# Kernel optimization log

Hardware: AMD Instinct MI355X
Metric: run time of the kernel (lower is better)

The kernel has to match this reference:

```python
import jax, jax.numpy as jnp
import numpy as np

ALPHA = 0.2  # LeakyReLU slope
NEG_INF = -9e15


def setup_inputs() -> dict:
    key = jax.random.key(0)
    ks = jax.random.split(key, 10)
    N, K, d = 20000, 32, 128
    R, S = 100, 4  # num relations, num domains
    item_embs = jax.random.normal(ks[0], (N, d), dtype=jnp.float32)
    entity_embs = jax.random.normal(ks[1], (N, K, d), dtype=jnp.float32)
    relations_embed = jax.random.normal(ks[2], (N, K, d), dtype=jnp.float32)
    relation_ids = jax.random.randint(ks[3], (N, K), 0, R, dtype=jnp.int32)
    adj_mask = jax.random.randint(ks[4], (N, K), 0, 2, dtype=jnp.int32)
    # fc_attention: Linear(3d, 1); out: Linear(d, d)
    fc_w = jax.random.normal(ks[5], (1, 3 * d), dtype=jnp.float32) * (1.0 / np.sqrt(3 * d))
    fc_b = jnp.zeros((1,), dtype=jnp.float32)
    out_w = jax.random.normal(ks[6], (d, d), dtype=jnp.float32) * (1.0 / np.sqrt(d))
    out_b = jnp.zeros((d,), dtype=jnp.float32)
    rel_dom_probs = jax.nn.softmax(jax.random.normal(ks[7], (R, S), dtype=jnp.float32), axis=-1)
    return {"item_embs": item_embs, "entity_embs": entity_embs,
            "relations_embed": relations_embed, "relation_ids": relation_ids,
            "adj_mask": adj_mask, "fc_w": fc_w, "fc_b": fc_b,
            "out_w": out_w, "out_b": out_b, "rel_dom_probs": rel_dom_probs}


def reference(item_embs, entity_embs, relations_embed, relation_ids, adj_mask,
              fc_w, fc_b, out_w, out_b, rel_dom_probs):
    N, K, d = entity_embs.shape
    R = rel_dom_probs.shape[0]
    # edge attention score: Linear(3d,1) on [item | relation | entity], then LeakyReLU
    Wh = jnp.broadcast_to(item_embs[:, None, :], (N, K, d))
    att_in = jnp.concatenate([Wh, relations_embed, entity_embs], axis=-1)  # [N,K,3d]
    e = jnp.einsum('nkf,of->nk', att_in, fc_w) + fc_b[0]
    e = jnp.where(e > 0, e, ALPHA * e)
    # masked softmax over neighbors (dropout inert in eval)
    masked = jnp.where(adj_mask > 0, e, NEG_INF)
    pi = jax.nn.softmax(masked, axis=1)  # [N,K]
    base = pi[..., None] * relations_embed * entity_embs  # [N,K,d]
    # domain-weighted aggregation: sum_s probs[rel_id, s], invalid ids -> 0
    valid = (relation_ids >= 0) & (relation_ids < R)
    safe_ids = jnp.clip(relation_ids, 0, R - 1)
    a_total = jnp.where(valid, rel_dom_probs[safe_ids].sum(-1), 0.0)  # [N,K]
    agg = jnp.einsum('nk,nkd->nd', a_total, base)  # [N,d]
    # residual + output Linear + ReLU
    out = (agg + item_embs) @ out_w.T + out_b
    return jax.nn.relu(out)
```

## Files before the change

kernel.cpp:

```cpp
#include <hip/hip_runtime.h>

#define ALPHA 0.2f
#define NEG_INF -9e15f

__device__ __forceinline__ void block_bar() {
    asm volatile("s_waitcnt lgkmcnt(0)" ::: "memory");
    __builtin_amdgcn_s_barrier();
}

__device__ __forceinline__ float dot4(float4 a, float4 b) {
    return a.x * b.x + a.y * b.y + a.z * b.z + a.w * b.w;
}

__global__ __launch_bounds__(256, 4)
void gat_k1(const float* __restrict__ item,
            const float* __restrict__ ent,
            const float* __restrict__ rel,
            const int*   __restrict__ rel_ids,
            const int*   __restrict__ adj,
            const float* __restrict__ fc_w,
            const float* __restrict__ fc_b,
            const float* __restrict__ probs,
            float* __restrict__ y,
            int N, int R)
{
    __shared__ __align__(16) float prod[2][4096];
    __shared__ float e_red[32];
    __shared__ float w_lds[32];
    __shared__ float sitem[2];
    __shared__ float asum[128];

    const int t = threadIdx.x;
    const int k = t >> 3, r = t & 7;
    const int base_off = k * 128 + r * 4;

    float4 fr[4], fe[4];
    #pragma unroll
    for (int c = 0; c < 4; ++c) {
        fr[c] = *(const float4*)&fc_w[128 + c * 32 + r * 4];
        fe[c] = *(const float4*)&fc_w[256 + c * 32 + r * 4];
    }
    const float fcw_i = (t < 128) ? fc_w[t] : 0.0f;
    const float fcb   = fc_b[0];
    if (t < R) {
        float4 q = *(const float4*)&probs[t * 4];
        asum[t] = q.x + q.y + q.z + q.w;
    }

    const int stride = gridDim.x;

    float4 pr[4], pe[4];
    float iv_p = 0.0f;
    int mv_p = 0, id_p = 0;
    {
        const float* rp  = rel + (size_t)blockIdx.x * 4096 + base_off;
        const float* epp = ent + (size_t)blockIdx.x * 4096 + base_off;
        #pragma unroll
        for (int c = 0; c < 4; ++c) {
            pr[c] = *(const float4*)(rp  + c * 32);
            pe[c] = *(const float4*)(epp + c * 32);
        }
        if (t < 128) iv_p = item[(size_t)blockIdx.x * 128 + t];
        if (t < 32) {
            mv_p = adj[(size_t)blockIdx.x * 32 + t];
            id_p = rel_ids[(size_t)blockIdx.x * 32 + t];
        }
    }

    int par = 0;
    for (int n = blockIdx.x; n < N; n += stride) {
        const float ivc = iv_p;
        const int mvc = mv_p, idc = id_p;

        float epa = 0.0f;
        float* pb = &prod[par][base_off];
        #pragma unroll
        for (int c = 0; c < 4; ++c) {
            float4 p;
            p.x = pr[c].x * pe[c].x;
            p.y = pr[c].y * pe[c].y;
            p.z = pr[c].z * pe[c].z;
            p.w = pr[c].w * pe[c].w;
            *(float4*)(pb + c * 32) = p;
            epa += dot4(pr[c], fr[c]) + dot4(pe[c], fe[c]);
        }

        int np = n + stride; if (np >= N) np = n;
        {
            const float* rp  = rel + (size_t)np * 4096 + base_off;
            const float* epp = ent + (size_t)np * 4096 + base_off;
            #pragma unroll
            for (int c = 0; c < 4; ++c) {
                pr[c] = *(const float4*)(rp  + c * 32);
                pe[c] = *(const float4*)(epp + c * 32);
            }
            if (t < 128) iv_p = item[(size_t)np * 128 + t];
            if (t < 32) {
                mv_p = adj[(size_t)np * 32 + t];
                id_p = rel_ids[(size_t)np * 32 + t];
            }
        }

        epa += __shfl_xor(epa, 1, 8);
        epa += __shfl_xor(epa, 2, 8);
        epa += __shfl_xor(epa, 4, 8);
        if (r == 0) e_red[k] = epa;
        if (t < 128) {
            float s = ivc * fcw_i;
            #pragma unroll
            for (int m = 1; m < 64; m <<= 1) s += __shfl_xor(s, m, 64);
            if ((t & 63) == 0) sitem[t >> 6] = s;
        }
        block_bar();

        if (t < 32) {
            float e = e_red[t] + sitem[0] + sitem[1] + fcb;
            e = (e > 0.0f) ? e : ALPHA * e;
            float m = (mvc > 0) ? e : NEG_INF;
            float mx = m;
            #pragma unroll
            for (int s2 = 16; s2 >= 1; s2 >>= 1) mx = fmaxf(mx, __shfl_xor(mx, s2, 32));
            float p = __expf(m - mx);
            float ps = p;
            #pragma unroll
            for (int s2 = 16; s2 >= 1; s2 >>= 1) ps += __shfl_xor(ps, s2, 32);
            float a = (idc >= 0 && idc < R) ? asum[idc] : 0.0f;
            w_lds[t] = (p / ps) * a;
        }
        block_bar();

        if (t < 128) {
            float s = 0.0f;
            const float* pp = &prod[par][t];
            #pragma unroll
            for (int kk = 0; kk < 32; ++kk) s = fmaf(w_lds[kk], pp[kk * 128], s);
            y[(size_t)n * 128 + t] = s + ivc;
        }
        par ^= 1;
    }
}

__global__ __launch_bounds__(256, 4)
void gat_k2(const float* __restrict__ out_w,
            const float* __restrict__ out_b,
            float* __restrict__ y, int N)
{
    __shared__ __align__(16) float ylds[128];
    __shared__ __align__(16) float plds[1024];

    const int t = threadIdx.x;
    const int c = t & 7;
    const int g = t >> 3;

    float4 w4[16];
    #pragma unroll
    for (int a = 0; a < 4; ++a)
        #pragma unroll
        for (int i = 0; i < 4; ++i)
            w4[a * 4 + i] = *(const float4*)&out_w[(size_t)(g * 4 + a) * 128 + c * 16 + i * 4];
    const float bj = out_b[t & 127];
    const int stride = gridDim.x;

    float vcur = 0.0f;
    if (t < 128) vcur = y[(size_t)blockIdx.x * 128 + t];

    for (int n = blockIdx.x; n < N; n += stride) {
        if (t < 128) ylds[t] = vcur;
        block_bar();
        int np = n + stride; if (np >= N) np = n;
        float vn = 0.0f;
        if (t < 128) vn = y[(size_t)np * 128 + t];

        float4 yc[4];
        #pragma unroll
        for (int i = 0; i < 4; ++i) yc[i] = *(const float4*)&ylds[c * 16 + i * 4];
        #pragma unroll
        for (int a = 0; a < 4; ++a) {
            float s = 0.0f;
            #pragma unroll
            for (int i = 0; i < 4; ++i) s += dot4(w4[a * 4 + i], yc[i]);
            plds[a * 256 + g * 8 + c] = s;
        }
        block_bar();
        if (t < 128) {
            const int j = t, a2 = j & 3, g2 = j >> 2;
            const float* pp = &plds[a2 * 256 + g2 * 8];
            float4 u0 = *(const float4*)pp;
            float4 u1 = *(const float4*)(pp + 4);
            float s = u0.x + u0.y + u0.z + u0.w + u1.x + u1.y + u1.z + u1.w + bj;
            y[(size_t)n * 128 + j] = fmaxf(s, 0.0f);
        }
        vcur = vn;
    }
}

extern "C" void kernel_launch(void* const* d_in, const int* in_sizes, int n_in,
                              void* d_out, int out_size, void* d_ws, size_t ws_size,
                              hipStream_t stream) {
    const float* item    = (const float*)d_in[0];
    const float* ent     = (const float*)d_in[1];
    const float* rel     = (const float*)d_in[2];
    const int*   rel_ids = (const int*)  d_in[3];
    const int*   adj     = (const int*)  d_in[4];
    const float* fc_w    = (const float*)d_in[5];
    const float* fc_b    = (const float*)d_in[6];
    const float* out_w   = (const float*)d_in[7];
    const float* out_b   = (const float*)d_in[8];
    const float* probs   = (const float*)d_in[9];
    float* out = (float*)d_out;

    const int N = in_sizes[0] / 128;
    const int R = in_sizes[9] / 4;

    int blocks1 = 2048; if (blocks1 > N) blocks1 = N;
    hipLaunchKernelGGL(gat_k1, dim3(blocks1), dim3(256), 0, stream,
                       item, ent, rel, rel_ids, adj, fc_w, fc_b, probs, out, N, R);

    int blocks2 = 2048; if (blocks2 > N) blocks2 = N;
    hipLaunchKernelGGL(gat_k2, dim3(blocks2), dim3(256), 0, stream,
                       out_w, out_b, out, N);
}
```

Before: 173.5 us.

## Map one wave per node in attention kernel, replacing block-wide barriers with shuffles

The first kernel changes from a persistent grid-stride loop, where each 256-thread block handled one node with LDS staging and two block barriers, to a non-persistent launch where each 64-lane wave owns one node. Each wave loads the whole 32x128 relation and entity tile into registers and reduces attention scores with shuffles. The neighbor-weighted sum is done in registers with lane broadcasts, and only a tiny per-wave LDS buffer with a wave-local fence remains. This removes block-level synchronisation and the LDS product buffer, at the cost of higher register pressure (launch bounds lowered to 3) and losing the explicit software prefetch of the next node.

After: 186.4 us. 7.4% more time.

```diff
diff --git a/kernel.cpp b/kernel.cpp
--- a/kernel.cpp
+++ b/kernel.cpp
@@ -3,16 +3,16 @@
 #define ALPHA 0.2f
 #define NEG_INF -9e15f
 
-__device__ __forceinline__ void block_bar() {
-    asm volatile("s_waitcnt lgkmcnt(0)" ::: "memory");
-    __builtin_amdgcn_s_barrier();
-}
-
 __device__ __forceinline__ float dot4(float4 a, float4 b) {
     return a.x * b.x + a.y * b.y + a.z * b.z + a.w * b.w;
 }
 
-__global__ __launch_bounds__(256, 4)
+__device__ __forceinline__ void wave_lds_fence() {
+    asm volatile("s_waitcnt lgkmcnt(0)" ::: "memory");
+    __builtin_amdgcn_sched_barrier(0);
+}
+
+__global__ __launch_bounds__(256, 3)
 void gat_k1(const float* __restrict__ item,
             const float* __restrict__ ent,
             const float* __restrict__ rel,
@@ -24,120 +24,112 @@
             float* __restrict__ y,
             int N, int R)
 {
-    __shared__ __align__(16) float prod[2][4096];
-    __shared__ float e_red[32];
-    __shared__ float w_lds[32];
-    __shared__ float sitem[2];
-    __shared__ float asum[128];
-
-    const int t = threadIdx.x;
-    const int k = t >> 3, r = t & 7;
-    const int base_off = k * 128 + r * 4;
-
-    float4 fr[4], fe[4];
-    #pragma unroll
-    for (int c = 0; c < 4; ++c) {
-        fr[c] = *(const float4*)&fc_w[128 + c * 32 + r * 4];
-        fe[c] = *(const float4*)&fc_w[256 + c * 32 + r * 4];
-    }
-    const float fcw_i = (t < 128) ? fc_w[t] : 0.0f;
-    const float fcb   = fc_b[0];
-    if (t < R) {
-        float4 q = *(const float4*)&probs[t * 4];
-        asum[t] = q.x + q.y + q.z + q.w;
-    }
-
-    const int stride = gridDim.x;
-
-    float4 pr[4], pe[4];
-    float iv_p = 0.0f;
-    int mv_p = 0, id_p = 0;
-    {
-        const float* rp  = rel + (size_t)blockIdx.x * 4096 + base_off;
-        const float* epp = ent + (size_t)blockIdx.x * 4096 + base_off;
-        #pragma unroll
-        for (int c = 0; c < 4; ++c) {
-            pr[c] = *(const float4*)(rp  + c * 32);
-            pe[c] = *(const float4*)(epp + c * 32);
+    __shared__ float e_lds[4][32];
+
+    const int t  = threadIdx.x;
+    const int wv = t >> 6;
+    const int l  = t & 63;
+    const int lh = l & 31;
+    const int hi = l >> 5;
+
+    const int n = blockIdx.x * 4 + wv;
+    if (n >= N) return;
+
+    const float4 fi = *(const float4*)&fc_w[4 * lh];
+    const float4 fr = *(const float4*)&fc_w[128 + 4 * lh];
+    const float4 fe = *(const float4*)&fc_w[256 + 4 * lh];
+    const float  fcb = fc_b[0];
+
+    const size_t nb = (size_t)n * 4096;
+    const float4 item4 = *(const float4*)&item[(size_t)n * 128 + 4 * lh];
+    const int    adjv  = adj[(size_t)n * 32 + lh];
+    const int    idv   = rel_ids[(size_t)n * 32 + lh];
+
+    const bool  valid = (idv >= 0) && (idv < R);
+    const int   sid   = valid ? idv : 0;
+    const float4 q    = *(const float4*)&probs[sid * 4];
+
+    float4 p[16];
+    float  ep[16];
+    #pragma unroll
+    for (int h = 0; h < 2; ++h) {
+        float4 rv[8], ev[8];
+        #pragma unroll
+        for (int c = 0; c < 8; ++c)
+            rv[c] = *(const float4*)&rel[nb + (h * 8 + c) * 256 + l * 4];
+        #pragma unroll
+        for (int c = 0; c < 8; ++c)
+            ev[c] = *(const float4*)&ent[nb + (h * 8 + c) * 256 + l * 4];
+        #pragma unroll
+        for (int c = 0; c < 8; ++c) {
+            const int cc = h * 8 + c;
+            float4 pp;
+            pp.x = rv[c].x * ev[c].x;
+            pp.y = rv[c].y * ev[c].y;
+            pp.z = rv[c].z * ev[c].z;
+            pp.w = rv[c].w * ev[c].w;
+            p[cc]  = pp;
+            ep[cc] = dot4(rv[c], fr) + dot4(ev[c], fe);
         }
-        if (t < 128) iv_p = item[(size_t)blockIdx.x * 128 + t];
-        if (t < 32) {
-            mv_p = adj[(size_t)blockIdx.x * 32 + t];
-            id_p = rel_ids[(size_t)blockIdx.x * 32 + t];
-        }
-    }
-
-    int par = 0;
-    for (int n = blockIdx.x; n < N; n += stride) {
-        const float ivc = iv_p;
-        const int mvc = mv_p, idc = id_p;
-
-        float epa = 0.0f;
-        float* pb = &prod[par][base_off];
-        #pragma unroll
-        for (int c = 0; c < 4; ++c) {
-            float4 p;
-            p.x = pr[c].x * pe[c].x;
-            p.y = pr[c].y * pe[c].y;
-            p.z = pr[c].z * pe[c].z;
-            p.w = pr[c].w * pe[c].w;
-            *(float4*)(pb + c * 32) = p;
-            epa += dot4(pr[c], fr[c]) + dot4(pe[c], fe[c]);
-        }
-
-        int np = n + stride; if (np >= N) np = n;
-        {
-            const float* rp  = rel + (size_t)np * 4096 + base_off;
-            const float* epp = ent + (size_t)np * 4096 + base_off;
-            #pragma unroll
-            for (int c = 0; c < 4; ++c) {
-                pr[c] = *(const float4*)(rp  + c * 32);
-                pe[c] = *(const float4*)(epp + c * 32);
-            }
-            if (t < 128) iv_p = item[(size_t)np * 128 + t];
-            if (t < 32) {
-                mv_p = adj[(size_t)np * 32 + t];
-                id_p = rel_ids[(size_t)np * 32 + t];
-            }
-        }
-
-        epa += __shfl_xor(epa, 1, 8);
-        epa += __shfl_xor(epa, 2, 8);
-        epa += __shfl_xor(epa, 4, 8);
-        if (r == 0) e_red[k] = epa;
-        if (t < 128) {
-            float s = ivc * fcw_i;
-            #pragma unroll
-            for (int m = 1; m < 64; m <<= 1) s += __shfl_xor(s, m, 64);
-            if ((t & 63) == 0) sitem[t >> 6] = s;
-        }
-        block_bar();
-
-        if (t < 32) {
-            float e = e_red[t] + sitem[0] + sitem[1] + fcb;
-            e = (e > 0.0f) ? e : ALPHA * e;
-            float m = (mvc > 0) ? e : NEG_INF;
-            float mx = m;
-            #pragma unroll
-            for (int s2 = 16; s2 >= 1; s2 >>= 1) mx = fmaxf(mx, __shfl_xor(mx, s2, 32));
-            float p = __expf(m - mx);
-            float ps = p;
-            #pragma unroll
-            for (int s2 = 16; s2 >= 1; s2 >>= 1) ps += __shfl_xor(ps, s2, 32);
-            float a = (idc >= 0 && idc < R) ? asum[idc] : 0.0f;
-            w_lds[t] = (p / ps) * a;
-        }
-        block_bar();
-
-        if (t < 128) {
-            float s = 0.0f;
-            const float* pp = &prod[par][t];
-            #pragma unroll
-            for (int kk = 0; kk < 32; ++kk) s = fmaf(w_lds[kk], pp[kk * 128], s);
-            y[(size_t)n * 128 + t] = s + ivc;
-        }
-        par ^= 1;
-    }
+    }
+
+    float sit = dot4(item4, fi);
+    #pragma unroll
+    for (int s = 16; s >= 1; s >>= 1) sit += __shfl_xor(sit, s, 32);
+
+    #pragma unroll
+    for (int c = 0; c < 16; ++c) {
+        float v = ep[c];
+        #pragma unroll
+        for (int s = 16; s >= 1; s >>= 1) v += __shfl_xor(v, s, 32);
+        ep[c] = v;
+    }
+    if (lh == 0) {
+        #pragma unroll
+        for (int c = 0; c < 16; ++c) e_lds[wv][2 * c + hi] = ep[c];
+    }
+    wave_lds_fence();
+
+    float em = e_lds[wv][lh] + sit + fcb;
+    em = (em > 0.0f) ? em : ALPHA * em;
+    float m = (adjv > 0) ? em : NEG_INF;
+    float mx = m;
+    #pragma unroll
+    for (int s = 16; s >= 1; s >>= 1) mx = fmaxf(mx, __shfl_xor(mx, s, 32));
+    float pe = __expf(m - mx);
+    float ps = pe;
+    #pragma unroll
+    for (int s = 16; s >= 1; s >>= 1) ps += __shfl_xor(ps, s, 32);
+    const float a  = valid ? (q.x + q.y + q.z + q.w) : 0.0f;
+    const float wk = (pe / ps) * a;
+
+    float4 acc = make_float4(0.f, 0.f, 0.f, 0.f);
+    #pragma unroll
+    for (int c = 0; c < 16; ++c) {
+        const float wc = __shfl(wk, 2 * c + hi, 64);
+        acc.x = fmaf(wc, p[c].x, acc.x);
+        acc.y = fmaf(wc, p[c].y, acc.y);
+        acc.z = fmaf(wc, p[c].z, acc.z);
+        acc.w = fmaf(wc, p[c].w, acc.w);
+    }
+    acc.x += __shfl_xor(acc.x, 32, 64);
+    acc.y += __shfl_xor(acc.y, 32, 64);
+    acc.z += __shfl_xor(acc.z, 32, 64);
+    acc.w += __shfl_xor(acc.w, 32, 64);
+
+    if (l < 32) {
+        float4 o;
+        o.x = acc.x + item4.x;
+        o.y = acc.y + item4.y;
+        o.z = acc.z + item4.z;
+        o.w = acc.w + item4.w;
+        *(float4*)&y[(size_t)n * 128 + 4 * lh] = o;
+    }
+}
+
+__device__ __forceinline__ void block_bar() {
+    asm volatile("s_waitcnt lgkmcnt(0)" ::: "memory");
+    __builtin_amdgcn_s_barrier();
 }
 
 __global__ __launch_bounds__(256, 4)
@@ -212,7 +204,7 @@
     const int N = in_sizes[0] / 128;
     const int R = in_sizes[9] / 4;
 
-    int blocks1 = 2048; if (blocks1 > N) blocks1 = N;
+    const int blocks1 = (N + 3) / 4;
     hipLaunchKernelGGL(gat_k1, dim3(blocks1), dim3(256), 0, stream,
                        item, ent, rel, rel_ids, adj, fc_w, fc_b, probs, out, N, R);
 
```
